# Optimization experiments

Hardware: AMD Instinct MI355X
Metric: run time of the kernel (lower is better)

## Reference

```python
import jax, jax.numpy as jnp
import numpy as np

B, S, D_IN, D_OUT = 4, 4096, 1024, 1024

def setup_inputs() -> dict:
    key = jax.random.key(0)
    kx, kq, kk, kv = jax.random.split(key, 4)
    x = jax.random.normal(kx, (B, S, D_IN), dtype=jnp.float32)
    # torch nn.Linear stores weight as [d_out, d_in]; y = x @ W.T
    Wq = jax.random.normal(kq, (D_OUT, D_IN), dtype=jnp.float32) * 0.02
    Wk = jax.random.normal(kk, (D_OUT, D_IN), dtype=jnp.float32) * 0.02
    Wv = jax.random.normal(kv, (D_OUT, D_IN), dtype=jnp.float32) * 0.02
    return {"x": x, "Wq": Wq, "Wk": Wk, "Wv": Wv}

def reference(x, Wq, Wk, Wv):
    b, n, _ = x.shape
    d_out = Wk.shape[0]
    q = jnp.einsum('bnd,od->bno', x, Wq)
    k = jnp.einsum('bnd,od->bno', x, Wk)
    v = jnp.einsum('bnd,od->bno', x, Wv)
    scores = jnp.einsum('bqo,bko->bqk', q, k)  # [B, S, S]
    causal = jnp.triu(jnp.ones((n, n), dtype=bool), k=1)
    scores = jnp.where(causal, -jnp.inf, scores)
    attn = jax.nn.softmax(scores / jnp.sqrt(jnp.float32(d_out)), axis=-1)
    # dropout p=0.0 -> identity
    return jnp.einsum('bqk,bko->bqo', attn, v)
```

## Files before the change

### kernel.cpp

```cpp
#include <hip/hip_runtime.h>


typedef unsigned short u16;
typedef unsigned int u32;
typedef __attribute__((ext_vector_type(8))) short bf16x8;
typedef __attribute__((ext_vector_type(4))) float f32x4;
typedef __attribute__((ext_vector_type(8))) unsigned short u16x8;

__device__ __forceinline__ u16 f2bf(float f) {
  union { float f; unsigned u; } v; v.f = f;
  unsigned r = v.u + 0x7FFFu + ((v.u >> 16) & 1u);
  return (u16)(r >> 16);
}
__device__ __forceinline__ float bf2f(u16 h) {
  union { unsigned u; float f; } v; v.u = ((unsigned)h) << 16;
  return v.f;
}
__device__ __forceinline__ f32x4 mfma16(bf16x8 a, bf16x8 b, f32x4 c) {
  return __builtin_amdgcn_mfma_f32_16x16x32_bf16(a, b, c, 0, 0, 0);
}
__device__ __forceinline__ void gld_lds16(const u16* g, u16* l) {
  __builtin_amdgcn_global_load_lds(
      (const __attribute__((address_space(1))) u32*)g,
      (__attribute__((address_space(3))) u32*)l, 16, 0, 0);
}
#define BAR() do { __builtin_amdgcn_s_barrier(); \
                   __builtin_amdgcn_sched_barrier(0); } while (0)
#define LGKM0() do { asm volatile("s_waitcnt lgkmcnt(0)" ::: "memory"); \
                     __builtin_amdgcn_sched_barrier(0); } while (0)
#define VMC(n) asm volatile("s_waitcnt vmcnt(" #n ")" ::: "memory")

__global__ __launch_bounds__(256)
void cast_all(const float* __restrict__ x, const float* __restrict__ Wq,
              const float* __restrict__ Wk, const float* __restrict__ Wv,
              u16* __restrict__ wX, u16* __restrict__ wWqkv) {
  int i = blockIdx.x * 256 + threadIdx.x;
  const float* src; u16* dst; int j;
  if (i < 2097152)        { src = x;  dst = wX;                j = i; }
  else if (i < 2228224)   { src = Wq; dst = wWqkv;             j = i - 2097152; }
  else if (i < 2359296)   { src = Wk; dst = wWqkv + 1048576;   j = i - 2228224; }
  else if (i < 2490368)   { src = Wv; dst = wWqkv + 2097152;   j = i - 2359296; }
  else return;
  const float4* s4 = (const float4*)src;
  float4 a = s4[2*j], b = s4[2*j+1];
  u16x8 o;
  o[0]=f2bf(a.x); o[1]=f2bf(a.y); o[2]=f2bf(a.z); o[3]=f2bf(a.w);
  o[4]=f2bf(b.x); o[5]=f2bf(b.y); o[6]=f2bf(b.z); o[7]=f2bf(b.w);
  ((u16x8*)dst)[j] = o;
}

#define GEMM8_CORE(Abase, Bbase)                                              \
  auto stageA = [&](int bufi, int h, int t) {                                 \
    _Pragma("unroll")                                                         \
    for (int i = 0; i < 2; ++i) {                                             \
      int ci = i * 512 + tid;                                                 \
      int r  = ci >> 3;                                                       \
      int c  = (ci & 7) ^ (r & 7);                                            \
      gld_lds16(Abase + (size_t)(h * 128 + r) * 1024 + t * 64 + c * 8,        \
                &At[bufi][h][ci * 8]);                                        \
    }                                                                         \
  };                                                                          \
  auto stageB = [&](int bufi, int h, int t) {                                 \
    _Pragma("unroll")                                                         \
    for (int i = 0; i < 2; ++i) {                                             \
      int ci = i * 512 + tid;                                                 \
      int r  = ci >> 3;                                                       \
      int c  = (ci & 7) ^ (r & 7);                                            \
      gld_lds16(Bbase + (size_t)(h * 128 + r) * 1024 + t * 64 + c * 8,        \
                &Bt[bufi][h][ci * 8]);                                        \
    }                                                                         \
  };                                                                          \
  bf16x8 af[8][2], bfr[4][2];                                                 \
  auto readA = [&](int bufi, int mb) {                                        \
    _Pragma("unroll")                                                         \
    for (int m = 0; m < 4; ++m)                                               \
      _Pragma("unroll")                                                       \
      for (int dk = 0; dk < 2; ++dk) {                                        \
        int r  = (mb + m) * 16 + c16;                                         \
        int ch = dk * 4 + g;                                                  \
        af[mb + m][dk] =                                                      \
            *(const bf16x8*)&At[bufi][wr][r * 64 + ((ch ^ (r & 7)) * 8)];     \
      }                                                                       \
  };                                                                          \
  auto readB = [&](int bufi, int nb) {                                        \
    _Pragma("unroll")                                                         \
    for (int n = 0; n < 2; ++n)                                               \
      _Pragma("unroll")                                                       \
      for (int dk = 0; dk < 2; ++dk) {                                        \
        int r  = (wc & 1) * 64 + (nb + n) * 16 + c16;                         \
        int ch = dk * 4 + g;                                                  \
        bfr[nb + n][dk] =                                                     \
            *(const bf16x8*)&Bt[bufi][wc >> 1][r * 64 + ((ch ^ (r & 7)) * 8)];\
      }                                                                       \
  };                                                                          \
  auto domfma = [&](int mb, int nb) {                                         \
    __builtin_amdgcn_s_setprio(1);                                            \
    _Pragma("unroll")                                                         \
    for (int dk = 0; dk < 2; ++dk)                                            \
      _Pragma("unroll")                                                       \
      for (int m = 0; m < 4; ++m)                                             \
        _Pragma("unroll")                                                     \
        for (int n = 0; n < 2; ++n)                                           \
          acc[mb + m][nb + n] =                                               \
              mfma16(af[mb + m][dk], bfr[nb + n][dk], acc[mb + m][nb + n]);   \
    __builtin_amdgcn_s_setprio(0);                                            \
  };                                                                          \
  stageA(0, 0, 0); stageA(0, 1, 0); stageB(0, 0, 0); stageB(0, 1, 0);         \
  stageA(1, 0, 1); stageA(1, 1, 1); stageB(1, 0, 1); stageB(1, 1, 1);         \
  VMC(8);                                                                     \
  BAR();                                                                      \
  for (int it = 0; it < 8; ++it) {                                            \
    const bool pf = (it < 7);                                                 \
    const int t2 = 2 * it + 2, t3 = 2 * it + 3;                               \
    readA(0, 0); readB(0, 0);                                                 \
    BAR(); LGKM0();                                                           \
    domfma(0, 0);                                                             \
    BAR();                                                                    \
    readA(0, 4);                                                              \
    BAR(); LGKM0();                                                           \
    domfma(4, 0);                                                             \
    BAR();                                                                    \
    readB(0, 2);                                                              \
    if (pf) { stageA(0, 0, t2); stageA(0, 1, t2); }                           \
    BAR(); LGKM0();                                                           \
    domfma(4, 2);                                                             \
    BAR();                                                                    \
    if (pf) { stageB(0, 0, t2); stageB(0, 1, t2); }                           \
    BAR();                                                                    \
    domfma(0, 2);                                                             \
    if (pf) { VMC(8); } else { VMC(0); }                                      \
    BAR();                                                                    \
    readA(1, 0); readB(1, 0);                                                 \
    BAR(); LGKM0();                                                           \
    domfma(0, 0);                                                             \
    BAR();                                                                    \
    readA(1, 4);                                                              \
    BAR(); LGKM0();                                                           \
    domfma(4, 0);                                                             \
    BAR();                                                                    \
    readB(1, 2);                                                              \
    if (pf) { stageA(1, 0, t3); stageA(1, 1, t3); }                           \
    BAR(); LGKM0();                                                           \
    domfma(4, 2);                                                             \
    BAR();                                                                    \
    if (pf) { stageB(1, 0, t3); stageB(1, 1, t3); }                           \
    BAR();                                                                    \
    domfma(0, 2);                                                             \
    if (pf) { VMC(8); } else { VMC(0); }                                      \
    BAR();                                                                    \
  }

__global__ __launch_bounds__(512, 1)
void qkv_gemm(const u16* __restrict__ X, const u16* __restrict__ W,
              u16* __restrict__ Qo, u16* __restrict__ Ko, u16* __restrict__ VTo) {
  __shared__ __align__(16) u16 At[2][2][128 * 64];
  __shared__ __align__(16) u16 Bt[2][2][128 * 64];
  const int tid = threadIdx.x;
  const int w = tid >> 6, lane = tid & 63;
  const int g = lane >> 4, c16 = lane & 15;
  const int wr = w >> 2, wc = w & 3;
  const int lid = blockIdx.x;
  const int xcd = lid & 7, gg = lid >> 3;
  const int M0 = ((xcd << 3) | (gg & 7)) * 256;
  const int N0 = (gg >> 3) * 256;
  const u16* Abase = X + (size_t)M0 * 1024;
  const u16* Bbase = W + (size_t)N0 * 1024;

  f32x4 acc[8][4] = {};
  GEMM8_CORE(Abase, Bbase);

  const int which = N0 >> 10;
  const int colbase = N0 & 1023;
#pragma unroll
  for (int m = 0; m < 8; ++m) {
#pragma unroll
    for (int n = 0; n < 4; ++n) {
#pragma unroll
      for (int r = 0; r < 4; ++r) {
        int gm  = M0 + wr * 128 + m * 16 + 4 * g + r;
        int col = colbase + wc * 64 + n * 16 + c16;
        u16 hv = f2bf(acc[m][n][r]);
        if (which == 0) {
          Qo[(size_t)gm * 1024 + col] = hv;
        } else if (which == 1) {
          Ko[(size_t)gm * 1024 + col] = hv;
        } else {
          int b = gm >> 12, s2 = gm & 4095;
          VTo[((size_t)((b << 10) + col)) * 4096 + s2] = hv;
        }
      }
    }
  }
}

__global__ __launch_bounds__(512, 1)
void sgemm_exp(const u16* __restrict__ Q, const u16* __restrict__ K,
               u16* __restrict__ Spack, float* __restrict__ lpart) {
  __shared__ __align__(16) u16 At[2][2][128 * 64];
  __shared__ __align__(16) u16 Bt[2][2][128 * 64];
  __shared__ float lsum[256][4];
  const int tid = threadIdx.x;
  const int w = tid >> 6, lane = tid & 63;
  const int g = lane >> 4, c16 = lane & 15;
  const int wr = w >> 2, wc = w & 3;
  const int b = blockIdx.y;

  int L = (blockIdx.x & 7) * 17 + (blockIdx.x >> 3);
  int qt = 0;
  while ((qt + 1) * (qt + 2) / 2 <= L) ++qt;
  const int kt = L - qt * (qt + 1) / 2;

  const u16* Abase = Q + (size_t)b * 4096 * 1024 + (size_t)qt * 256 * 1024;
  const u16* Bbase = K + (size_t)b * 4096 * 1024 + (size_t)kt * 256 * 1024;

  f32x4 acc[8][4] = {};
  GEMM8_CORE(Abase, Bbase);

  const int qt128 = 2 * qt + wr;
  const int kt128 = 2 * kt + (wc >> 1);
  const bool exists = (kt128 <= qt128);
  u16* Sb = Spack + (((size_t)b * 528 + (size_t)(qt128 * (qt128 + 1)) / 2 + kt128) << 14);
  const int q0 = qt * 256, k0g = kt * 256;
  float psum[8][4];
#pragma unroll
  for (int m = 0; m < 8; ++m)
#pragma unroll
    for (int r = 0; r < 4; ++r) psum[m][r] = 0.f;
#pragma unroll
  for (int m = 0; m < 8; ++m) {
#pragma unroll
    for (int n = 0; n < 4; ++n) {
#pragma unroll
      for (int r = 0; r < 4; ++r) {
        int rl = wr * 128 + m * 16 + 4 * g + r;
        int cl = wc * 64 + n * 16 + c16;
        float s = acc[m][n][r] * 0.03125f;
        float p = (k0g + cl <= q0 + rl) ? __expf(s) : 0.f;
        u16 pb = f2bf(p);
        if (exists) Sb[(rl & 127) * 128 + (cl & 127)] = pb;
        psum[m][r] += bf2f(pb);
      }
    }
  }
#pragma unroll
  for (int m = 0; m < 8; ++m)
#pragma unroll
    for (int r = 0; r < 4; ++r) {
      float v = psum[m][r];
      v += __shfl_xor(v, 1, 64);
      v += __shfl_xor(v, 2, 64);
      v += __shfl_xor(v, 4, 64);
      v += __shfl_xor(v, 8, 64);
      psum[m][r] = v;
    }
  if (c16 == 0) {
#pragma unroll
    for (int m = 0; m < 8; ++m)
#pragma unroll
      for (int r = 0; r < 4; ++r)
        lsum[wr * 128 + m * 16 + 4 * g + r][wc] = psum[m][r];
  }
  __syncthreads();
  if (tid < 256) {
    float v = lsum[tid][0] + lsum[tid][1] + lsum[tid][2] + lsum[tid][3];
    lpart[((size_t)b * 4096 + q0 + tid) * 16 + kt] = v;
  }
}

__global__ __launch_bounds__(512, 1)
void pv_gemm(const u16* __restrict__ Spack, const u16* __restrict__ VT,
             const u16* __restrict__ ztile, const float* __restrict__ lpart,
             float* __restrict__ Out) {
  __shared__ __align__(16) u16 At[2][256 * 64];
  __shared__ __align__(16) u16 Bt[2][128 * 64];
  __shared__ float linv_lds[512];
  const int tid = threadIdx.x;
  const int w = tid >> 6, lane = tid & 63;
  const int g = lane >> 4, c16 = lane & 15;
  const int wm = w >> 1, wn = w & 1;
  const int pp = blockIdx.x;
  const int d0 = blockIdx.y;
  const int b  = blockIdx.z;

  const u16* Sp_b = Spack + (size_t)b * 528 * 16384;
  const u16* VTb  = VT + (size_t)b * 1024 * 4096;
  float* Ob = Out + (size_t)b * 4096 * 1024;

  {
    const int QTr = (tid < 256) ? pp : (15 - pp);
    const int row = QTr * 256 + (tid & 255);
    const int nt  = QTr + 1;
    const float* p = lpart + ((size_t)b * 4096 + row) * 16;
    float s = 0.f;
    for (int i = 0; i < nt; ++i) s += p[i];
    linv_lds[tid] = 1.f / s;
  }

  for (int pass = 0; pass < 2; ++pass) {
    const int QT = pass == 0 ? pp : 15 - pp;
    const int M0 = QT * 256;
    const int nsteps = (QT + 1) * 4;
    const int niter  = nsteps >> 1;
    const int tLo = 2 * QT;
    const size_t triLo = (size_t)(tLo * (tLo + 1)) / 2;
    const size_t triHi = (size_t)((tLo + 1) * (tLo + 2)) / 2;

    f32x4 acc[4][4] = {};

    auto stA = [&](int bufi, int half, int tt) {
      const int kt128 = tt >> 1;
      const int koff = (tt & 1) * 64;
      const u16* base;
      if (half == 0) base = (kt128 <= tLo) ? Sp_b + ((triLo + kt128) << 14) : ztile;
      else           base = Sp_b + ((triHi + kt128) << 14);
#pragma unroll
      for (int i = 0; i < 2; ++i) {
        int ci = (half * 2 + i) * 512 + tid;
        int r = ci >> 3;
        int c = (ci & 7) ^ (r & 7);
        gld_lds16(base + (size_t)(r & 127) * 128 + koff + c * 8, &At[bufi][ci * 8]);
      }
    };
    auto stB = [&](int bufi, int tt) {
      const int kv0 = tt * 64;
#pragma unroll
      for (int i = 0; i < 2; ++i) {
        int ci = i * 512 + tid;
        int r = ci >> 3;
        int c = (ci & 7) ^ (r & 7);
        gld_lds16(VTb + (size_t)(d0 * 128 + r) * 4096 + kv0 + c * 8, &Bt[bufi][ci * 8]);
      }
    };

    bf16x8 af[4][2], bfr[4][2];
    auto readA = [&](int bufi, int mb) {
#pragma unroll
      for (int m = 0; m < 2; ++m)
#pragma unroll
        for (int dk = 0; dk < 2; ++dk) {
          int row = wm * 64 + (mb + m) * 16 + c16;
          int ch = dk * 4 + g;
          af[mb + m][dk] = *(const bf16x8*)&At[bufi][row * 64 + ((ch ^ (row & 7)) * 8)];
        }
    };
    auto readB = [&](int bufi, int nb) {
#pragma unroll
      for (int n = 0; n < 2; ++n)
#pragma unroll
        for (int dk = 0; dk < 2; ++dk) {
          int row = wn * 64 + (nb + n) * 16 + c16;
          int ch = dk * 4 + g;
          bfr[nb + n][dk] = *(const bf16x8*)&Bt[bufi][row * 64 + ((ch ^ (row & 7)) * 8)];
        }
    };
    auto domfma = [&](int mb, int nb) {
      __builtin_amdgcn_s_setprio(1);
#pragma unroll
      for (int dk = 0; dk < 2; ++dk)
#pragma unroll
        for (int m = 0; m < 2; ++m)
#pragma unroll
          for (int n = 0; n < 2; ++n)
            acc[mb + m][nb + n] = mfma16(af[mb + m][dk], bfr[nb + n][dk], acc[mb + m][nb + n]);
      __builtin_amdgcn_s_setprio(0);
    };

    stA(0, 0, 0); stA(0, 1, 0); stB(0, 0);
    stA(1, 0, 1); stA(1, 1, 1); stB(1, 1);
    VMC(6);
    BAR();
    for (int it = 0; it < niter; ++it) {
      const bool pf = (it + 1 < niter);
      const int t2 = 2 * it + 2, t3 = 2 * it + 3;
      readA(0, 0); readB(0, 0);
      BAR(); LGKM0();
      domfma(0, 0);
      BAR();
      readA(0, 2);
      BAR(); LGKM0();
      domfma(2, 0);
      BAR();
      readB(0, 2);
      if (pf) { stA(0, 0, t2); stA(0, 1, t2); }
      BAR(); LGKM0();
      domfma(2, 2);
      BAR();
      if (pf) stB(0, t2);
      BAR();
      domfma(0, 2);
      if (pf) { VMC(6); } else { VMC(0); }
      BAR();
      readA(1, 0); readB(1, 0);
      BAR(); LGKM0();
      domfma(0, 0);
      BAR();
      readA(1, 2);
      BAR(); LGKM0();
      domfma(2, 0);
      BAR();
      readB(1, 2);
      if (pf) { stA(1, 0, t3); stA(1, 1, t3); }
      BAR(); LGKM0();
      domfma(2, 2);
      BAR();
      if (pf) stB(1, t3);
      BAR();
      domfma(0, 2);
      if (pf) { VMC(6); } else { VMC(0); }
      BAR();
    }

    const float* lb = linv_lds + pass * 256;
#pragma unroll
    for (int m = 0; m < 4; ++m) {
#pragma unroll
      for (int r = 0; r < 4; ++r) {
        int rl = wm * 64 + m * 16 + 4 * g + r;
        float li = lb[rl];
#pragma unroll
        for (int n = 0; n < 4; ++n) {
          int dcol = d0 * 128 + wn * 64 + n * 16 + c16;
          Ob[(size_t)(M0 + rl) * 1024 + dcol] = acc[m][n][r] * li;
        }
      }
    }
  }
}

__global__ __launch_bounds__(512, 2)
void attn_kernel(const u16* __restrict__ Q, const u16* __restrict__ K,
                 const u16* __restrict__ VT, float* __restrict__ Out) {
  __shared__ u16 kv_lds[32 * 1024];
  __shared__ float s_part[4][32][33];
  __shared__ u16 p_lds[32 * 40];
  __shared__ float l_lds[32];

  const int tid = threadIdx.x;
  const int w = tid >> 6, lane = tid & 63;
  const int g = lane >> 4, c16 = lane & 15;
  const int b  = blockIdx.x & 3;
  const int qb = 127 - (blockIdx.x >> 2);
  const int qs = qb * 32;
  const int kh = w & 1, dq = w >> 1;

  const u16* Qb  = Q  + (size_t)b * 4096 * 1024;
  const u16* Kb  = K  + (size_t)b * 4096 * 1024;
  const u16* VTb = VT + (size_t)b * 1024 * 4096;

  bf16x8 qfrag[2][8];
#pragma unroll
  for (int qh = 0; qh < 2; ++qh)
#pragma unroll
    for (int dk = 0; dk < 8; ++dk)
      qfrag[qh][dk] = *(const bf16x8*)(Qb + (size_t)(qs + qh * 16 + c16) * 1024
                                       + dq * 256 + dk * 32 + g * 8);

  f32x4 oacc[2][8] = {};
  if (tid < 32) l_lds[tid] = 0.f;

  const int qrow_p = tid >> 4;
  const int kk     = tid & 15;
  const int gq     = qs + qrow_p;

  for (int j = 0; j <= qb; ++j) {
    const int kv0 = j * 32;
    __syncthreads();
    uint4 rk[8];
#pragma unroll
    for (int i = 0; i < 8; ++i) {
      int ci = i * 512 + tid;
      int r  = ci >> 7;
      int c  = (ci & 127) ^ (r & 7);
      rk[i] = *(const uint4*)(Kb + (size_t)(kv0 + r) * 1024 + c * 8);
    }
#pragma unroll
    for (int i = 0; i < 8; ++i)
      *(uint4*)&kv_lds[(size_t)(i * 512 + tid) * 8] = rk[i];
    __syncthreads();
    f32x4 sacc[2] = {};
#pragma unroll
    for (int dk = 0; dk < 8; ++dk) {
      int kvrow = kh * 16 + c16;
      int ch    = dq * 32 + dk * 4 + g;
      bf16x8 kf = *(const bf16x8*)&kv_lds[kvrow * 1024 + ((ch ^ (kvrow & 7)) * 8)];
      sacc[0] = mfma16(qfrag[0][dk], kf, sacc[0]);
      sacc[1] = mfma16(qfrag[1][dk], kf, sacc[1]);
    }
#pragma unroll
    for (int qh = 0; qh < 2; ++qh)
#pragma unroll
      for (int r = 0; r < 4; ++r)
        s_part[dq][qh * 16 + 4 * g + r][kh * 16 + c16] = sacc[qh][r];
    __syncthreads();
    uint4 rv[8];
#pragma unroll
    for (int i = 0; i < 8; ++i) {
      int ci = i * 512 + tid;
      int d  = ((ci >> 6) << 4) + (ci & 15);
      int c  = (ci >> 4) & 3;
      rv[i] = *(const uint4*)(VTb + (size_t)d * 4096 + kv0 + c * 8);
    }
    {
      float psum = 0.f;
#pragma unroll
      for (int h = 0; h < 2; ++h) {
        int kcol = kk + h * 16;
        float s = s_part[0][qrow_p][kcol] + s_part[1][qrow_p][kcol]
                + s_part[2][qrow_p][kcol] + s_part[3][qrow_p][kcol];
        s *= 0.03125f;
        float p = (kv0 + kcol <= gq) ? __expf(s) : 0.f;
        u16 pb = f2bf(p);
        p_lds[qrow_p * 40 + kcol] = pb;
        psum += bf2f(pb);
      }
#pragma unroll
      for (int off = 1; off < 16; off <<= 1)
        psum += __shfl_xor(psum, off, 64);
      if (kk == 0) l_lds[qrow_p] += psum;
    }
#pragma unroll
    for (int i = 0; i < 8; ++i)
      *(uint4*)&kv_lds[(size_t)(i * 512 + tid) * 8] = rv[i];
    __syncthreads();
    bf16x8 pa0 = *(const bf16x8*)&p_lds[(0  + c16) * 40 + g * 8];
    bf16x8 pa1 = *(const bf16x8*)&p_lds[(16 + c16) * 40 + g * 8];
#pragma unroll
    for (int f = 0; f < 8; ++f) {
      int dcol = w * 128 + f * 16 + c16;
      int pos  = (dcol >> 4) * 64 + g * 16 + (dcol & 15);
      bf16x8 vf = *(const bf16x8*)&kv_lds[(size_t)pos * 8];
      oacc[0][f] = mfma16(pa0, vf, oacc[0][f]);
      oacc[1][f] = mfma16(pa1, vf, oacc[1][f]);
    }
  }

  float* Ob = Out + (size_t)b * 4096 * 1024;
#pragma unroll
  for (int qh = 0; qh < 2; ++qh) {
#pragma unroll
    for (int r = 0; r < 4; ++r) {
      int ql = qh * 16 + 4 * g + r;
      float linvv = 1.f / l_lds[ql];
#pragma unroll
      for (int f = 0; f < 8; ++f)
        Ob[(size_t)(qs + ql) * 1024 + w * 128 + f * 16 + c16] = oacc[qh][f][r] * linvv;
    }
  }
}

extern "C" void kernel_launch(void* const* d_in, const int* in_sizes, int n_in,
                              void* d_out, int out_size, void* d_ws, size_t ws_size,
                              hipStream_t stream) {
  const float* x  = (const float*)d_in[0];
  const float* Wq = (const float*)d_in[1];
  const float* Wk = (const float*)d_in[2];
  const float* Wv = (const float*)d_in[3];
  float* out = (float*)d_out;

  u16* ws    = (u16*)d_ws;
  u16* wWqkv = ws;
  u16* wX    = wWqkv + (size_t)3 * 1024 * 1024;
  u16* wQ    = wX + (size_t)16384 * 1024;
  u16* wK    = wQ + (size_t)16384 * 1024;
  u16* wVT   = wK + (size_t)16384 * 1024;
  u16* wSp   = wVT + (size_t)16384 * 1024;
  float* lpart = (float*)(ws + (size_t)104857600);

  cast_all<<<dim3(9728), 256, 0, stream>>>(x, Wq, Wk, Wv, wX, wWqkv);

  qkv_gemm<<<dim3(768), 512, 0, stream>>>(wX, wWqkv, wQ, wK, wVT);

  if (ws_size >= (size_t)211877888) {
    hipMemsetAsync(wX, 0, 32768, stream);
    sgemm_exp<<<dim3(136, 4), 512, 0, stream>>>(wQ, wK, wSp, lpart);
    pv_gemm<<<dim3(8, 8, 4), 512, 0, stream>>>(wSp, wVT, wX, lpart, out);
  } else {
    attn_kernel<<<dim3(512), 512, 0, stream>>>(wQ, wK, wVT, out);
  }
}
```

Measured before the change: 356.1 us.

## Shrink QKV and score GEMM tiles to 256x128 with simpler double buffering

Replaces the hand-scheduled 256x256, K=64 GEMM core with a 256x128 tile, K=32 double-buffered loop used by both the QKV projection and the score/exp kernel. Launch bounds move from 1 to 4 blocks per CU and grid sizes double. The score kernel now works on 128-wide key tiles and writes 32 partial row sums per row instead of 16, and pv_gemm reads that new layout. The aim is more resident blocks to hide latency and finer causal tile granularity. The cost is less data reuse per tile and the loss of the interleaved read/MFMA/prefetch schedule with setprio.

```diff
diff --git a/kernel.cpp b/kernel.cpp
--- a/kernel.cpp
+++ b/kernel.cpp
@@ -49,136 +49,79 @@
   ((u16x8*)dst)[j] = o;
 }
 
-#define GEMM8_CORE(Abase, Bbase)                                              \
-  auto stageA = [&](int bufi, int h, int t) {                                 \
+#define GEMM_CO_CORE(Abase, Bbase)                                            \
+  auto stage = [&](int s, int k0) {                                           \
     _Pragma("unroll")                                                         \
     for (int i = 0; i < 2; ++i) {                                             \
-      int ci = i * 512 + tid;                                                 \
-      int r  = ci >> 3;                                                       \
-      int c  = (ci & 7) ^ (r & 7);                                            \
-      gld_lds16(Abase + (size_t)(h * 128 + r) * 1024 + t * 64 + c * 8,        \
-                &At[bufi][h][ci * 8]);                                        \
+      int ci = i * 512 + tid;                              \
+      int r  = ci >> 2;                                                       \
+      int c  = (ci & 3) ^ ((r >> 1) & 3);                                     \
+      gld_lds16(Abase + (size_t)r * 1024 + k0 + c * 8, &At[s][ci * 8]);       \
+    }                                                                         \
+    {                                                                         \
+      int ci = tid;                                         \
+      int r  = ci >> 2;                                                       \
+      int c  = (ci & 3) ^ ((r >> 1) & 3);                                     \
+      gld_lds16(Bbase + (size_t)r * 1024 + k0 + c * 8, &Bt[s][ci * 8]);       \
     }                                                                         \
   };                                                                          \
-  auto stageB = [&](int bufi, int h, int t) {                                 \
+  auto compute = [&](int s) {                                                 \
+    bf16x8 af[4], bfr[4];                                                     \
     _Pragma("unroll")                                                         \
-    for (int i = 0; i < 2; ++i) {                                             \
-      int ci = i * 512 + tid;                                                 \
-      int r  = ci >> 3;                                                       \
-      int c  = (ci & 7) ^ (r & 7);                                            \
-      gld_lds16(Bbase + (size_t)(h * 128 + r) * 1024 + t * 64 + c * 8,        \
-                &Bt[bufi][h][ci * 8]);                                        \
+    for (int m = 0; m < 4; ++m) {                                             \
+      int row = wm * 64 + m * 16 + c16;                                       \
+      af[m] = *(const bf16x8*)&At[s][row * 32 + ((g ^ ((row >> 1) & 3)) * 8)];\
     }                                                                         \
-  };                                                                          \
-  bf16x8 af[8][2], bfr[4][2];                                                 \
-  auto readA = [&](int bufi, int mb) {                                        \
+    _Pragma("unroll")                                                         \
+    for (int n = 0; n < 4; ++n) {                                             \
+      int row = wn * 64 + n * 16 + c16;                                       \
+      bfr[n] = *(const bf16x8*)&Bt[s][row * 32 + ((g ^ ((row >> 1) & 3)) * 8)];\
+    }                                                                         \
     _Pragma("unroll")                                                         \
     for (int m = 0; m < 4; ++m)                                               \
       _Pragma("unroll")                                                       \
-      for (int dk = 0; dk < 2; ++dk) {                                        \
-        int r  = (mb + m) * 16 + c16;                                         \
-        int ch = dk * 4 + g;                                                  \
-        af[mb + m][dk] =                                                      \
-            *(const bf16x8*)&At[bufi][wr][r * 64 + ((ch ^ (r & 7)) * 8)];     \
-      }                                                                       \
+      for (int n = 0; n < 4; ++n)                                             \
+        acc[m][n] = mfma16(af[m], bfr[n], acc[m][n]);                         \
   };                                                                          \
-  auto readB = [&](int bufi, int nb) {                                        \
-    _Pragma("unroll")                                                         \
-    for (int n = 0; n < 2; ++n)                                               \
-      _Pragma("unroll")                                                       \
-      for (int dk = 0; dk < 2; ++dk) {                                        \
-        int r  = (wc & 1) * 64 + (nb + n) * 16 + c16;                         \
-        int ch = dk * 4 + g;                                                  \
-        bfr[nb + n][dk] =                                                     \
-            *(const bf16x8*)&Bt[bufi][wc >> 1][r * 64 + ((ch ^ (r & 7)) * 8)];\
-      }                                                                       \
-  };                                                                          \
-  auto domfma = [&](int mb, int nb) {                                         \
-    __builtin_amdgcn_s_setprio(1);                                            \
-    _Pragma("unroll")                                                         \
-    for (int dk = 0; dk < 2; ++dk)                                            \
-      _Pragma("unroll")                                                       \
-      for (int m = 0; m < 4; ++m)                                             \
-        _Pragma("unroll")                                                     \
-        for (int n = 0; n < 2; ++n)                                           \
-          acc[mb + m][nb + n] =                                               \
-              mfma16(af[mb + m][dk], bfr[nb + n][dk], acc[mb + m][nb + n]);   \
-    __builtin_amdgcn_s_setprio(0);                                            \
-  };                                                                          \
-  stageA(0, 0, 0); stageA(0, 1, 0); stageB(0, 0, 0); stageB(0, 1, 0);         \
-  stageA(1, 0, 1); stageA(1, 1, 1); stageB(1, 0, 1); stageB(1, 1, 1);         \
-  VMC(8);                                                                     \
-  BAR();                                                                      \
-  for (int it = 0; it < 8; ++it) {                                            \
-    const bool pf = (it < 7);                                                 \
-    const int t2 = 2 * it + 2, t3 = 2 * it + 3;                               \
-    readA(0, 0); readB(0, 0);                                                 \
-    BAR(); LGKM0();                                                           \
-    domfma(0, 0);                                                             \
-    BAR();                                                                    \
-    readA(0, 4);                                                              \
-    BAR(); LGKM0();                                                           \
-    domfma(4, 0);                                                             \
-    BAR();                                                                    \
-    readB(0, 2);                                                              \
-    if (pf) { stageA(0, 0, t2); stageA(0, 1, t2); }                           \
-    BAR(); LGKM0();                                                           \
-    domfma(4, 2);                                                             \
-    BAR();                                                                    \
-    if (pf) { stageB(0, 0, t2); stageB(0, 1, t2); }                           \
-    BAR();                                                                    \
-    domfma(0, 2);                                                             \
-    if (pf) { VMC(8); } else { VMC(0); }                                      \
-    BAR();                                                                    \
-    readA(1, 0); readB(1, 0);                                                 \
-    BAR(); LGKM0();                                                           \
-    domfma(0, 0);                                                             \
-    BAR();                                                                    \
-    readA(1, 4);                                                              \
-    BAR(); LGKM0();                                                           \
-    domfma(4, 0);                                                             \
-    BAR();                                                                    \
-    readB(1, 2);                                                              \
-    if (pf) { stageA(1, 0, t3); stageA(1, 1, t3); }                           \
-    BAR(); LGKM0();                                                           \
-    domfma(4, 2);                                                             \
-    BAR();                                                                    \
-    if (pf) { stageB(1, 0, t3); stageB(1, 1, t3); }                           \
-    BAR();                                                                    \
-    domfma(0, 2);                                                             \
-    if (pf) { VMC(8); } else { VMC(0); }                                      \
-    BAR();                                                                    \
-  }
-
-__global__ __launch_bounds__(512, 1)
+  stage(0, 0);                                                                \
+  __syncthreads();                                                            \
+  int cur = 0;                                                                \
+  for (int t = 0; t < 32; ++t) {                                              \
+    if (t < 31) stage(cur ^ 1, (t + 1) * 32);                                 \
+    compute(cur);                                                             \
+    __syncthreads();                                                          \
+    cur ^= 1;                                                                 \
+  }
+
+__global__ __launch_bounds__(512, 4)
 void qkv_gemm(const u16* __restrict__ X, const u16* __restrict__ W,
               u16* __restrict__ Qo, u16* __restrict__ Ko, u16* __restrict__ VTo) {
-  __shared__ __align__(16) u16 At[2][2][128 * 64];
-  __shared__ __align__(16) u16 Bt[2][2][128 * 64];
+  __shared__ __align__(16) u16 At[2][256 * 32];
+  __shared__ __align__(16) u16 Bt[2][128 * 32];
   const int tid = threadIdx.x;
   const int w = tid >> 6, lane = tid & 63;
   const int g = lane >> 4, c16 = lane & 15;
-  const int wr = w >> 2, wc = w & 3;
+  const int wm = w >> 1, wn = w & 1;
   const int lid = blockIdx.x;
   const int xcd = lid & 7, gg = lid >> 3;
   const int M0 = ((xcd << 3) | (gg & 7)) * 256;
-  const int N0 = (gg >> 3) * 256;
+  const int N0 = (gg >> 3) * 128;
   const u16* Abase = X + (size_t)M0 * 1024;
   const u16* Bbase = W + (size_t)N0 * 1024;
 
-  f32x4 acc[8][4] = {};
-  GEMM8_CORE(Abase, Bbase);
+  f32x4 acc[4][4] = {};
+  GEMM_CO_CORE(Abase, Bbase);
 
   const int which = N0 >> 10;
   const int colbase = N0 & 1023;
 #pragma unroll
-  for (int m = 0; m < 8; ++m) {
+  for (int m = 0; m < 4; ++m) {
 #pragma unroll
     for (int n = 0; n < 4; ++n) {
 #pragma unroll
       for (int r = 0; r < 4; ++r) {
-        int gm  = M0 + wr * 128 + m * 16 + 4 * g + r;
-        int col = colbase + wc * 64 + n * 16 + c16;
+        int gm  = M0 + wm * 64 + m * 16 + 4 * g + r;
+        int col = colbase + wn * 64 + n * 16 + c16;
         u16 hv = f2bf(acc[m][n][r]);
         if (which == 0) {
           Qo[(size_t)gm * 1024 + col] = hv;
@@ -193,57 +136,56 @@
   }
 }
 
-__global__ __launch_bounds__(512, 1)
+__global__ __launch_bounds__(512, 4)
 void sgemm_exp(const u16* __restrict__ Q, const u16* __restrict__ K,
                u16* __restrict__ Spack, float* __restrict__ lpart) {
-  __shared__ __align__(16) u16 At[2][2][128 * 64];
-  __shared__ __align__(16) u16 Bt[2][2][128 * 64];
-  __shared__ float lsum[256][4];
+  __shared__ __align__(16) u16 At[2][256 * 32];
+  __shared__ __align__(16) u16 Bt[2][128 * 32];
+  __shared__ float lsum[256][2];
   const int tid = threadIdx.x;
   const int w = tid >> 6, lane = tid & 63;
   const int g = lane >> 4, c16 = lane & 15;
-  const int wr = w >> 2, wc = w & 3;
+  const int wm = w >> 1, wn = w & 1;
   const int b = blockIdx.y;
 
-  int L = (blockIdx.x & 7) * 17 + (blockIdx.x >> 3);
+  int L = (blockIdx.x & 7) * 34 + (blockIdx.x >> 3);
   int qt = 0;
-  while ((qt + 1) * (qt + 2) / 2 <= L) ++qt;
-  const int kt = L - qt * (qt + 1) / 2;
+  while ((qt + 1) * (qt + 2) <= L) ++qt;
+  const int kt128 = L - qt * (qt + 1);
 
   const u16* Abase = Q + (size_t)b * 4096 * 1024 + (size_t)qt * 256 * 1024;
-  const u16* Bbase = K + (size_t)b * 4096 * 1024 + (size_t)kt * 256 * 1024;
-
-  f32x4 acc[8][4] = {};
-  GEMM8_CORE(Abase, Bbase);
-
-  const int qt128 = 2 * qt + wr;
-  const int kt128 = 2 * kt + (wc >> 1);
+  const u16* Bbase = K + (size_t)b * 4096 * 1024 + (size_t)kt128 * 128 * 1024;
+
+  f32x4 acc[4][4] = {};
+  GEMM_CO_CORE(Abase, Bbase);
+
+  const int qt128 = 2 * qt + (wm >> 1);
   const bool exists = (kt128 <= qt128);
   u16* Sb = Spack + (((size_t)b * 528 + (size_t)(qt128 * (qt128 + 1)) / 2 + kt128) << 14);
-  const int q0 = qt * 256, k0g = kt * 256;
-  float psum[8][4];
-#pragma unroll
-  for (int m = 0; m < 8; ++m)
+  const int q0 = qt * 256, k0g = kt128 * 128;
+  float psum[4][4];
+#pragma unroll
+  for (int m = 0; m < 4; ++m)
 #pragma unroll
     for (int r = 0; r < 4; ++r) psum[m][r] = 0.f;
 #pragma unroll
-  for (int m = 0; m < 8; ++m) {
+  for (int m = 0; m < 4; ++m) {
 #pragma unroll
     for (int n = 0; n < 4; ++n) {
 #pragma unroll
       for (int r = 0; r < 4; ++r) {
-        int rl = wr * 128 + m * 16 + 4 * g + r;
-        int cl = wc * 64 + n * 16 + c16;
+        int rl = wm * 64 + m * 16 + 4 * g + r;
+        int cl = wn * 64 + n * 16 + c16;
         float s = acc[m][n][r] * 0.03125f;
         float p = (k0g + cl <= q0 + rl) ? __expf(s) : 0.f;
         u16 pb = f2bf(p);
-        if (exists) Sb[(rl & 127) * 128 + (cl & 127)] = pb;
+        if (exists) Sb[(rl & 127) * 128 + cl] = pb;
         psum[m][r] += bf2f(pb);
       }
     }
   }
 #pragma unroll
-  for (int m = 0; m < 8; ++m)
+  for (int m = 0; m < 4; ++m)
 #pragma unroll
     for (int r = 0; r < 4; ++r) {
       float v = psum[m][r];
@@ -255,15 +197,15 @@
     }
   if (c16 == 0) {
 #pragma unroll
-    for (int m = 0; m < 8; ++m)
+    for (int m = 0; m < 4; ++m)
 #pragma unroll
       for (int r = 0; r < 4; ++r)
-        lsum[wr * 128 + m * 16 + 4 * g + r][wc] = psum[m][r];
+        lsum[wm * 64 + m * 16 + 4 * g + r][wn] = psum[m][r];
   }
   __syncthreads();
   if (tid < 256) {
-    float v = lsum[tid][0] + lsum[tid][1] + lsum[tid][2] + lsum[tid][3];
-    lpart[((size_t)b * 4096 + q0 + tid) * 16 + kt] = v;
+    float v = lsum[tid][0] + lsum[tid][1];
+    lpart[((size_t)b * 4096 + q0 + tid) * 32 + kt128] = v;
   }
 }
 
@@ -289,8 +231,8 @@
   {
     const int QTr = (tid < 256) ? pp : (15 - pp);
     const int row = QTr * 256 + (tid & 255);
-    const int nt  = QTr + 1;
-    const float* p = lpart + ((size_t)b * 4096 + row) * 16;
+    const int nt  = 2 * QTr + 1 + ((tid >> 7) & 1);
+    const float* p = lpart + ((size_t)b * 4096 + row) * 32;
     float s = 0.f;
     for (int i = 0; i < nt; ++i) s += p[i];
     linv_lds[tid] = 1.f / s;
@@ -568,11 +510,11 @@
 
   cast_all<<<dim3(9728), 256, 0, stream>>>(x, Wq, Wk, Wv, wX, wWqkv);
 
-  qkv_gemm<<<dim3(768), 512, 0, stream>>>(wX, wWqkv, wQ, wK, wVT);
+  qkv_gemm<<<dim3(1536), 512, 0, stream>>>(wX, wWqkv, wQ, wK, wVT);
 
   if (ws_size >= (size_t)211877888) {
     hipMemsetAsync(wX, 0, 32768, stream);
-    sgemm_exp<<<dim3(136, 4), 512, 0, stream>>>(wQ, wK, wSp, lpart);
+    sgemm_exp<<<dim3(272, 4), 512, 0, stream>>>(wQ, wK, wSp, lpart);
     pv_gemm<<<dim3(8, 8, 4), 512, 0, stream>>>(wSp, wVT, wX, lpart, out);
   } else {
     attn_kernel<<<dim3(512), 512, 0, stream>>>(wQ, wK, wVT, out);
```

New measurement: 360.1 us. Within noise of the previous version (+1.1%).
